# Optimization experiments

Hardware: AMD Instinct MI355X
Metric: run time of the kernel (lower is better)

The kernel has to match this reference:

```python
import jax, jax.numpy as jnp
import numpy as np

N_QUBITS = 5
N_LAYERS = 3
DIM = 2 ** N_QUBITS  # 32


def _apply_ry(state, theta, w):
    # state: [B, 32] complex64; theta: scalar or [B] float32
    half = theta * 0.5
    c = jnp.cos(half)
    s = jnp.sin(half)
    if c.ndim:  # per-sample angles
        c = c[:, None, None]
        s = s[:, None, None]
    pre, post = 2 ** w, 2 ** (N_QUBITS - 1 - w)
    st = state.reshape(-1, pre, 2, post)
    s0, s1 = st[:, :, 0, :], st[:, :, 1, :]
    out = jnp.stack([c * s0 - s * s1, s * s0 + c * s1], axis=2)
    return out.reshape(-1, DIM)


def _apply_rz(state, theta, w):
    half = theta * 0.5
    e0 = jnp.exp(-1j * half)
    e1 = jnp.exp(1j * half)
    pre, post = 2 ** w, 2 ** (N_QUBITS - 1 - w)
    st = state.reshape(-1, pre, 2, post)
    out = jnp.stack([e0 * st[:, :, 0, :], e1 * st[:, :, 1, :]], axis=2)
    return out.reshape(-1, DIM)


def _apply_cnot(state, c):
    # control wire c, target wire c+1 (adjacent, as in the CNOT chain)
    pre, post = 2 ** c, 2 ** (N_QUBITS - 2 - c)
    st = state.reshape(-1, pre, 2, 2, post)
    out = jnp.stack([st[:, :, 0], st[:, :, 1, ::-1, :]], axis=2)
    return out.reshape(-1, DIM)


def _expval_z(state, w):
    pre, post = 2 ** w, 2 ** (N_QUBITS - 1 - w)
    p = jnp.abs(state.reshape(-1, pre, 2, post)) ** 2
    return (p[:, :, 0, :] - p[:, :, 1, :]).sum(axis=(1, 2))


def _circuit(enc, qp):
    # enc: [B, 5] in [-1,1]; qp: [30]
    B = enc.shape[0]
    state = jnp.zeros((B, DIM), jnp.complex64).at[:, 0].set(1.0)
    pi = jnp.float32(np.pi)
    for i in range(N_QUBITS):
        state = _apply_ry(state, enc[:, i] * pi, i)
    idx = 0
    for _ in range(N_LAYERS):
        for i in range(N_QUBITS):
            state = _apply_ry(state, qp[idx], i); idx += 1
            state = _apply_rz(state, qp[idx], i); idx += 1
        for i in range(N_QUBITS - 1):
            state = _apply_cnot(state, i)
    return jnp.stack([_expval_z(state, i) for i in range(N_QUBITS)], axis=1)


def setup_inputs() -> dict:
    key = jax.random.key(0)
    ks = jax.random.split(key, 14)
    B, S, A = 131072, 252, 4
    def lin(k, fin, fout):
        return jax.random.normal(k, (fin, fout), jnp.float32) / jnp.sqrt(jnp.float32(fin))
    return {
        'state': jax.random.normal(ks[0], (B, S), jnp.float32),
        'W1': lin(ks[1], S, 128), 'b1': jnp.zeros((128,), jnp.float32),
        'W2': lin(ks[2], 128, 64), 'b2': jnp.zeros((64,), jnp.float32),
        'W3': lin(ks[3], 64, N_QUBITS), 'b3': jnp.zeros((N_QUBITS,), jnp.float32),
        'qp': jax.random.normal(ks[4], (N_LAYERS * N_QUBITS * 2,), jnp.float32) * 0.1,
        'D1': lin(ks[5], N_QUBITS, 32), 'd1': jnp.zeros((32,), jnp.float32),
        'D2': lin(ks[6], 32, 16), 'd2': jnp.zeros((16,), jnp.float32),
        'D3': lin(ks[7], 16, A), 'd3': jnp.zeros((A,), jnp.float32),
    }


def reference(state, W1, b1, W2, b2, W3, b3, qp, D1, d1, D2, d2, D3, d3):
    h = jax.nn.relu(state @ W1 + b1)
    h = jax.nn.relu(h @ W2 + b2)
    enc = jnp.tanh(h @ W3 + b3)          # [B, 5]
    q = _circuit(enc, qp)                # [B, 5] PauliZ expectations
    h = jax.nn.relu(q @ D1 + d1)
    h = jax.nn.relu(h @ D2 + d2)
    return h @ D3 + d3                   # [B, action_dim]
```

## Files before the change

kernel.cpp:

```cpp
#include <hip/hip_runtime.h>
#include <hip/hip_bf16.h>
#include <math.h>

typedef _Float16 half8_t __attribute__((ext_vector_type(8)));
typedef _Float16 half4_t __attribute__((ext_vector_type(4)));
typedef float floatx4 __attribute__((ext_vector_type(4)));

#define TPT 8

__device__ __forceinline__ void lds_barrier() {
    asm volatile("s_waitcnt lgkmcnt(0)" ::: "memory");
    __builtin_amdgcn_s_barrier();
    asm volatile("" ::: "memory");
}

__device__ __forceinline__ float fast_tanh(float x) {
    float e = __expf(2.f * x);
    return 1.f - 2.f / (e + 1.f);
}

__device__ __forceinline__ void prep_body(const float* __restrict__ W,
                                          _Float16* __restrict__ dst,
                                          int K, int N, int KS, int b) {
    int ks   = b % KS;
    int nt   = b / KS;
    int lane = threadIdx.x;
    int col  = nt * 16 + (lane & 15);
    int kbase = ks * 32 + ((lane >> 4) << 3);
    half8_t v;
#pragma unroll
    for (int j = 0; j < 8; ++j) {
        int k = kbase + j;
        float x = (k < K && col < N) ? W[(size_t)k * N + col] : 0.f;
        v[j] = (_Float16)x;
    }
    *(half8_t*)(dst + (size_t)(b * 64 + lane) * 8) = v;
}

__global__ void prep_all(const float* __restrict__ W1, const float* __restrict__ W2,
                         const float* __restrict__ W3,
                         _Float16* __restrict__ w1f, _Float16* __restrict__ w2f,
                         _Float16* __restrict__ w3f) {
    int b = blockIdx.x;
    if (b < 64)      prep_body(W1, w1f, 252, 128, 8, b);
    else if (b < 80) prep_body(W2, w2f, 128, 64, 4, b - 64);
    else             prep_body(W3, w3f, 64, 5, 2, b - 80);
}

__global__ __launch_bounds__(512, 4) void front_kernel(
    const float* __restrict__ state,
    const _Float16* __restrict__ w1f, const float* __restrict__ b1,
    const _Float16* __restrict__ w2f, const float* __restrict__ b2,
    const _Float16* __restrict__ w3f, const float* __restrict__ b3,
    float* __restrict__ enc, int Btot) {
    __shared__ char lds[63488];
    const int tid = threadIdx.x;
    const int w   = tid >> 6;
    const int l   = tid & 63;
    const int l15 = l & 15;
    const int lhi = l >> 4;
    const int row0 = blockIdx.x * (32 * TPT);

    const int srow = tid >> 4;
    const int sc0  = tid & 15;
    const int sswz = (srow & 7) << 4;

    floatx4 pf[4];

#define ISSUE_A(T)                                                          \
    {                                                                       \
        const float* Ar = state + (size_t)(row0 + (T) * 32 + srow) * 252;   \
        _Pragma("unroll")                                                   \
        for (int jj = 0; jj < 4; ++jj) {                                    \
            int c = sc0 + jj * 16;                                          \
            if (c < 63) pf[jj] = *(const floatx4*)(Ar + c * 4);             \
        }                                                                   \
    }

#define STAGE(T)                                                            \
    {                                                                       \
        int sab = (((T) & 1) << 14);                                        \
        _Pragma("unroll")                                                   \
        for (int jj = 0; jj < 4; ++jj) {                                    \
            int c = sc0 + jj * 16;                                          \
            half4_t h;                                                      \
            if (c == 63) {                                                  \
                h = half4_t{0, 0, 0, 0};                                    \
            } else {                                                        \
                floatx4 f = pf[jj];                                         \
                h = half4_t{ (_Float16)f[0], (_Float16)f[1],                \
                             (_Float16)f[2], (_Float16)f[3] };              \
            }                                                               \
            *(half4_t*)(lds + sab + (srow << 9) + ((c * 8) ^ sswz)) = h;    \
        }                                                                   \
    }

    ISSUE_A(0)

    half8_t bw1[8];
#pragma unroll
    for (int ks = 0; ks < 8; ++ks)
        bw1[ks] = *(const half8_t*)(w1f + (size_t)((w * 8 + ks) * 64 + l) * 8);

    {
        const floatx4* s2 = (const floatx4*)w2f;
        *(floatx4*)(lds + 45056 + tid * 16)        = s2[tid];
        *(floatx4*)(lds + 45056 + 8192 + tid * 16) = s2[512 + tid];
        if (tid < 128) {
            const floatx4* s3 = (const floatx4*)w3f;
            *(floatx4*)(lds + 61440 + tid * 16) = s3[tid];
        }
    }

    const float bb1 = b1[w * 16 + l15];
    const float bb2 = b2[(w & 3) * 16 + l15];
    const float bb3 = b3[l15 < 5 ? l15 : 4];

    const int mi2 = w >> 2;
    const int nt2 = w & 3;

    STAGE(0)
    ISSUE_A(1)
    lds_barrier();

#pragma unroll
    for (int t = 0; t < TPT; ++t) {
        if (w < 2 && t > 0) {
            floatx4 acc3 = floatx4{0, 0, 0, 0};
#pragma unroll
            for (int ks = 0; ks < 2; ++ks) {
                int r = w * 16 + l15;
                int cb = ks * 64 + lhi * 16;
                half8_t a  = *(const half8_t*)(lds + 40960 + (r << 7) + (cb ^ ((r & 7) << 4)));
                half8_t bf = *(const half8_t*)(lds + 61440 + (ks * 64 + l) * 16);
                acc3 = __builtin_amdgcn_mfma_f32_16x16x32_f16(a, bf, acc3, 0, 0, 0);
            }
            if (l15 < 5) {
#pragma unroll
                for (int ri = 0; ri < 4; ++ri) {
                    int grow = row0 + (t - 1) * 32 + w * 16 + lhi * 4 + ri;
                    enc[(size_t)l15 * Btot + grow] = fast_tanh(acc3[ri] + bb3);
                }
            }
        }

        const int sab = (t & 1) << 14;
        floatx4 acc1[2] = { floatx4{0, 0, 0, 0}, floatx4{0, 0, 0, 0} };
#pragma unroll
        for (int ks = 0; ks < 8; ++ks) {
            int cb = ks * 64 + lhi * 16;
#pragma unroll
            for (int mi = 0; mi < 2; ++mi) {
                int r = mi * 16 + l15;
                half8_t a = *(const half8_t*)(lds + sab + (r << 9) + (cb ^ ((r & 7) << 4)));
                acc1[mi] = __builtin_amdgcn_mfma_f32_16x16x32_f16(a, bw1[ks], acc1[mi], 0, 0, 0);
            }
        }

        {
            int col2 = (w * 16 + l15) * 2;
#pragma unroll
            for (int mi = 0; mi < 2; ++mi)
#pragma unroll
                for (int ri = 0; ri < 4; ++ri) {
                    int row = mi * 16 + lhi * 4 + ri;
                    float v = acc1[mi][ri] + bb1;
                    v = v > 0.f ? v : 0.f;
                    *(_Float16*)(lds + 32768 + (row << 8) + (col2 ^ ((row & 7) << 4))) = (_Float16)v;
                }
        }
        lds_barrier();

        floatx4 acc2 = floatx4{0, 0, 0, 0};
#pragma unroll
        for (int ks = 0; ks < 4; ++ks) {
            int r = mi2 * 16 + l15;
            int cb = ks * 64 + lhi * 16;
            half8_t a  = *(const half8_t*)(lds + 32768 + (r << 8) + (cb ^ ((r & 7) << 4)));
            half8_t bf = *(const half8_t*)(lds + 45056 + ((nt2 * 4 + ks) * 64 + l) * 16);
            acc2 = __builtin_amdgcn_mfma_f32_16x16x32_f16(a, bf, acc2, 0, 0, 0);
        }

        {
            int col2 = (nt2 * 16 + l15) * 2;
#pragma unroll
            for (int ri = 0; ri < 4; ++ri) {
                int row = mi2 * 16 + lhi * 4 + ri;
                float v = acc2[ri] + bb2;
                v = v > 0.f ? v : 0.f;
                *(_Float16*)(lds + 40960 + (row << 7) + (col2 ^ ((row & 7) << 4))) = (_Float16)v;
            }
        }

        if (t + 1 < TPT) {
            STAGE(t + 1)
            if (t + 2 < TPT) ISSUE_A(t + 2)
        }
        lds_barrier();
    }

    if (w < 2) {
        floatx4 acc3 = floatx4{0, 0, 0, 0};
#pragma unroll
        for (int ks = 0; ks < 2; ++ks) {
            int r = w * 16 + l15;
            int cb = ks * 64 + lhi * 16;
            half8_t a  = *(const half8_t*)(lds + 40960 + (r << 7) + (cb ^ ((r & 7) << 4)));
            half8_t bf = *(const half8_t*)(lds + 61440 + (ks * 64 + l) * 16);
            acc3 = __builtin_amdgcn_mfma_f32_16x16x32_f16(a, bf, acc3, 0, 0, 0);
        }
        if (l15 < 5) {
#pragma unroll
            for (int ri = 0; ri < 4; ++ri) {
                int grow = row0 + (TPT - 1) * 32 + w * 16 + lhi * 4 + ri;
                enc[(size_t)l15 * Btot + grow] = fast_tanh(acc3[ri] + bb3);
            }
        }
    }
#undef ISSUE_A
#undef STAGE
}

template<int P>
__device__ __forceinline__ void ry_g(float* re, float* im, float c, float s) {
    constexpr int STR = 1 << P;
#pragma unroll
    for (int base = 0; base < 32; base += 2 * STR)
#pragma unroll
        for (int d = 0; d < STR; ++d) {
            int i0 = base + d, i1 = i0 + STR;
            float r0 = re[i0], r1 = re[i1], m0 = im[i0], m1 = im[i1];
            re[i0] = c * r0 - s * r1;  re[i1] = s * r0 + c * r1;
            im[i0] = c * m0 - s * m1;  im[i1] = s * m0 + c * m1;
        }
}

template<int P>
__device__ __forceinline__ void rz_g(float* re, float* im, float c, float s) {
#pragma unroll
    for (int i = 0; i < 32; ++i) {
        float t = ((i >> P) & 1) ? s : -s;
        float r = re[i], m = im[i];
        re[i] = c * r - t * m;
        im[i] = c * m + t * r;
    }
}

template<int PC, int PT>
__device__ __forceinline__ void cnot_g(float* re, float* im) {
#pragma unroll
    for (int i = 0; i < 32; ++i) {
        if (((i >> PC) & 1) && !((i >> PT) & 1)) {
            int j = i | (1 << PT);
            float t;
            t = re[i]; re[i] = re[j]; re[j] = t;
            t = im[i]; im[i] = im[j]; im[j] = t;
        }
    }
}

template<int P>
__device__ __forceinline__ void expand_g(float* re, float* im,
                                         float arv, float aiv, float brv, float biv) {
#pragma unroll
    for (int base = 0; base < 32; base += (2 << P)) {
        float cr = re[base], ci = im[base];
        re[base + (1 << P)] = cr * brv - ci * biv;
        im[base + (1 << P)] = cr * biv + ci * brv;
        re[base] = cr * arv - ci * aiv;
        im[base] = cr * aiv + ci * arv;
    }
}

__global__ __launch_bounds__(256) void back_kernel(
    const float* __restrict__ enc, const float* __restrict__ qp,
    const float* __restrict__ D1, const float* __restrict__ d1,
    const float* __restrict__ D2, const float* __restrict__ d2,
    const float* __restrict__ D3, const float* __restrict__ d3,
    float* __restrict__ out, int Btot) {
    __shared__ float sD1[160], sd1[32], sD2[512], sd2[16], sD3[64], sd3[4];
    __shared__ float sQc[20], sQs[20];
    __shared__ float ryh[5], rzc0[5], rzs0[5];
    const int tid = threadIdx.x;
    for (int i = tid; i < 512; i += 256) sD2[i] = D2[i];
    if (tid < 160) sD1[tid] = D1[tid];
    if (tid < 32)  sd1[tid] = d1[tid];
    if (tid < 64)  sD3[tid] = D3[tid];
    if (tid < 16)  sd2[tid] = d2[tid];
    if (tid < 4)   sd3[tid] = d3[tid];
    if (tid < 20) { float h = 0.5f * qp[10 + tid]; sQc[tid] = __cosf(h); sQs[tid] = __sinf(h); }
    if (tid < 5) {
        ryh[tid] = 0.5f * qp[2 * tid];
        float h = 0.5f * qp[2 * tid + 1];
        rzc0[tid] = __cosf(h);
        rzs0[tid] = __sinf(h);
    }
    __syncthreads();

    const size_t r = (size_t)blockIdx.x * 256 + tid;

    const float HPI = 1.57079632679489662f;
    float ar[5], ai[5], br[5], bi[5];
#pragma unroll
    for (int i = 0; i < 5; ++i) {
        float h = enc[(size_t)i * Btot + r] * HPI + ryh[i];
        float ch = __cosf(h), sh = __sinf(h);
        ar[i] = ch * rzc0[i];  ai[i] = -ch * rzs0[i];
        br[i] = sh * rzc0[i];  bi[i] =  sh * rzs0[i];
    }

    float re[32], im[32];
    re[0] = ar[0]; im[0] = ai[0]; re[16] = br[0]; im[16] = bi[0];
    expand_g<3>(re, im, ar[1], ai[1], br[1], bi[1]);
    expand_g<2>(re, im, ar[2], ai[2], br[2], bi[2]);
    expand_g<1>(re, im, ar[3], ai[3], br[3], bi[3]);
    expand_g<0>(re, im, ar[4], ai[4], br[4], bi[4]);

    cnot_g<4, 3>(re, im);
    cnot_g<3, 2>(re, im);
    cnot_g<2, 1>(re, im);
    cnot_g<1, 0>(re, im);

#pragma unroll
    for (int lay = 0; lay < 2; ++lay) {
        const float* c = sQc + lay * 10;
        const float* s = sQs + lay * 10;
        ry_g<4>(re, im, c[0], s[0]);  rz_g<4>(re, im, c[1], s[1]);
        ry_g<3>(re, im, c[2], s[2]);  rz_g<3>(re, im, c[3], s[3]);
        ry_g<2>(re, im, c[4], s[4]);  rz_g<2>(re, im, c[5], s[5]);
        ry_g<1>(re, im, c[6], s[6]);  rz_g<1>(re, im, c[7], s[7]);
        ry_g<0>(re, im, c[8], s[8]);  rz_g<0>(re, im, c[9], s[9]);
        cnot_g<4, 3>(re, im);
        cnot_g<3, 2>(re, im);
        cnot_g<2, 1>(re, im);
        cnot_g<1, 0>(re, im);
    }

    float q[5] = {0, 0, 0, 0, 0};
#pragma unroll
    for (int i = 0; i < 32; ++i) {
        float p = re[i] * re[i] + im[i] * im[i];
        q[0] += ((i >> 4) & 1) ? -p : p;
        q[1] += ((i >> 3) & 1) ? -p : p;
        q[2] += ((i >> 2) & 1) ? -p : p;
        q[3] += ((i >> 1) & 1) ? -p : p;
        q[4] += ( i       & 1) ? -p : p;
    }

    float h1[32];
#pragma unroll
    for (int j = 0; j < 32; ++j) {
        float a = sd1[j];
#pragma unroll
        for (int k = 0; k < 5; ++k) a += q[k] * sD1[k * 32 + j];
        h1[j] = a > 0.f ? a : 0.f;
    }
    float h2[16];
#pragma unroll
    for (int j = 0; j < 16; ++j) {
        float a = sd2[j];
#pragma unroll
        for (int k = 0; k < 32; ++k) a += h1[k] * sD2[k * 16 + j];
        h2[j] = a > 0.f ? a : 0.f;
    }
    floatx4 o;
#pragma unroll
    for (int j = 0; j < 4; ++j) {
        float a = sd3[j];
#pragma unroll
        for (int k = 0; k < 16; ++k) a += h2[k] * sD3[k * 4 + j];
        o[j] = a;
    }
    *(floatx4*)(out + r * 4) = o;
}

extern "C" void kernel_launch(void* const* d_in, const int* in_sizes, int n_in,
                              void* d_out, int out_size, void* d_ws, size_t ws_size,
                              hipStream_t stream) {
    const float* state = (const float*)d_in[0];
    const float* W1 = (const float*)d_in[1];
    const float* b1 = (const float*)d_in[2];
    const float* W2 = (const float*)d_in[3];
    const float* b2 = (const float*)d_in[4];
    const float* W3 = (const float*)d_in[5];
    const float* b3 = (const float*)d_in[6];
    const float* qp = (const float*)d_in[7];
    const float* D1 = (const float*)d_in[8];
    const float* d1 = (const float*)d_in[9];
    const float* D2 = (const float*)d_in[10];
    const float* d2 = (const float*)d_in[11];
    const float* D3 = (const float*)d_in[12];
    const float* d3 = (const float*)d_in[13];
    float* out = (float*)d_out;

    const int B = in_sizes[0] / 252;

    char* ws = (char*)d_ws;
    _Float16* w1f = (_Float16*)ws;
    _Float16* w2f = (_Float16*)(ws + 65536);
    _Float16* w3f = (_Float16*)(ws + 65536 + 16384);
    float*    enc = (float*)(ws + 65536 + 16384 + 2048);

    prep_all<<<82, 64, 0, stream>>>(W1, W2, W3, w1f, w2f, w3f);
    front_kernel<<<B / (32 * TPT), 512, 0, stream>>>(state, w1f, b1, w2f, b2, w3f, b3, enc, B);
    back_kernel<<<B / 256, 256, 0, stream>>>(enc, qp, D1, d1, D2, d2, D3, d3, out, B);
}
```

Before: 54.64 us.

## Fuse weight prep, front MLP, circuit and decoder into one kernel

```diff
diff --git a/kernel.cpp b/kernel.cpp
--- a/kernel.cpp
+++ b/kernel.cpp
@@ -19,41 +19,82 @@
     return 1.f - 2.f / (e + 1.f);
 }
 
-__device__ __forceinline__ void prep_body(const float* __restrict__ W,
-                                          _Float16* __restrict__ dst,
-                                          int K, int N, int KS, int b) {
-    int ks   = b % KS;
-    int nt   = b / KS;
-    int lane = threadIdx.x;
-    int col  = nt * 16 + (lane & 15);
-    int kbase = ks * 32 + ((lane >> 4) << 3);
-    half8_t v;
-#pragma unroll
-    for (int j = 0; j < 8; ++j) {
-        int k = kbase + j;
-        float x = (k < K && col < N) ? W[(size_t)k * N + col] : 0.f;
-        v[j] = (_Float16)x;
-    }
-    *(half8_t*)(dst + (size_t)(b * 64 + lane) * 8) = v;
-}
-
-__global__ void prep_all(const float* __restrict__ W1, const float* __restrict__ W2,
-                         const float* __restrict__ W3,
-                         _Float16* __restrict__ w1f, _Float16* __restrict__ w2f,
-                         _Float16* __restrict__ w3f) {
-    int b = blockIdx.x;
-    if (b < 64)      prep_body(W1, w1f, 252, 128, 8, b);
-    else if (b < 80) prep_body(W2, w2f, 128, 64, 4, b - 64);
-    else             prep_body(W3, w3f, 64, 5, 2, b - 80);
-}
-
-__global__ __launch_bounds__(512, 4) void front_kernel(
+template<int P>
+__device__ __forceinline__ void ry_g(float* re, float* im, float c, float s) {
+    constexpr int STR = 1 << P;
+#pragma unroll
+    for (int base = 0; base < 32; base += 2 * STR)
+#pragma unroll
+        for (int d = 0; d < STR; ++d) {
+            int i0 = base + d, i1 = i0 + STR;
+            float r0 = re[i0], r1 = re[i1], m0 = im[i0], m1 = im[i1];
+            re[i0] = c * r0 - s * r1;  re[i1] = s * r0 + c * r1;
+            im[i0] = c * m0 - s * m1;  im[i1] = s * m0 + c * m1;
+        }
+}
+template<int P>
+__device__ __forceinline__ void rz_g(float* re, float* im, float c, float s) {
+#pragma unroll
+    for (int i = 0; i < 32; ++i) {
+        float t = ((i >> P) & 1) ? s : -s;
+        float r = re[i], m = im[i];
+        re[i] = c * r - t * m;
+        im[i] = c * m + t * r;
+    }
+}
+template<int PC, int PT>
+__device__ __forceinline__ void cnot_g(float* re, float* im) {
+#pragma unroll
+    for (int i = 0; i < 32; ++i) {
+        if (((i >> PC) & 1) && !((i >> PT) & 1)) {
+            int j = i | (1 << PT);
+            float t;
+            t = re[i]; re[i] = re[j]; re[j] = t;
+            t = im[i]; im[i] = im[j]; im[j] = t;
+        }
+    }
+}
+template<int P>
+__device__ __forceinline__ void expand_g(float* re, float* im,
+                                         float arv, float aiv, float brv, float biv) {
+#pragma unroll
+    for (int base = 0; base < 32; base += (2 << P)) {
+        float cr = re[base], ci = im[base];
+        re[base + (1 << P)] = cr * brv - ci * biv;
+        im[base + (1 << P)] = cr * biv + ci * brv;
+        re[base] = cr * arv - ci * aiv;
+        im[base] = cr * aiv + ci * arv;
+    }
+}
+
+#define OF_H1   32768
+#define OF_H2   40960
+#define OF_ENC  45056
+#define OF_D1   50176
+#define OF_d1   50816
+#define OF_D2   50944
+#define OF_d2   52992
+#define OF_D3   53056
+#define OF_d3   53312
+#define OF_RYH  53328
+#define OF_RZC  53348
+#define OF_RZS  53368
+#define OF_QC   53392
+#define OF_QS   53472
+
+__global__ __launch_bounds__(512, 4) void fused_kernel(
     const float* __restrict__ state,
-    const _Float16* __restrict__ w1f, const float* __restrict__ b1,
-    const _Float16* __restrict__ w2f, const float* __restrict__ b2,
-    const _Float16* __restrict__ w3f, const float* __restrict__ b3,
-    float* __restrict__ enc, int Btot) {
-    __shared__ char lds[63488];
+    const float* __restrict__ W1, const float* __restrict__ b1,
+    const float* __restrict__ W2, const float* __restrict__ b2,
+    const float* __restrict__ W3, const float* __restrict__ b3,
+    const float* __restrict__ qp,
+    const float* __restrict__ D1, const float* __restrict__ d1,
+    const float* __restrict__ D2, const float* __restrict__ d2,
+    const float* __restrict__ D3, const float* __restrict__ d3,
+    float* __restrict__ out) {
+    __shared__ floatx4 ldsv[3348];
+    char*  lds  = (char*)ldsv;
+    float* ldsf = (float*)ldsv;
     const int tid = threadIdx.x;
     const int w   = tid >> 6;
     const int l   = tid & 63;
@@ -97,27 +138,65 @@
 
     ISSUE_A(0)
 
+    const int nt2 = w & 3;
+    const int mi2 = w >> 2;
+
     half8_t bw1[8];
 #pragma unroll
-    for (int ks = 0; ks < 8; ++ks)
-        bw1[ks] = *(const half8_t*)(w1f + (size_t)((w * 8 + ks) * 64 + l) * 8);
-
-    {
-        const floatx4* s2 = (const floatx4*)w2f;
-        *(floatx4*)(lds + 45056 + tid * 16)        = s2[tid];
-        *(floatx4*)(lds + 45056 + 8192 + tid * 16) = s2[512 + tid];
-        if (tid < 128) {
-            const floatx4* s3 = (const floatx4*)w3f;
-            *(floatx4*)(lds + 61440 + tid * 16) = s3[tid];
-        }
+    for (int ks = 0; ks < 8; ++ks) {
+        half8_t v;
+#pragma unroll
+        for (int j = 0; j < 8; ++j) {
+            int k = ks * 32 + lhi * 8 + j;
+            float x = (k < 252) ? W1[k * 128 + w * 16 + l15] : 0.f;
+            v[j] = (_Float16)x;
+        }
+        bw1[ks] = v;
+    }
+    half8_t bw2[4];
+#pragma unroll
+    for (int ks = 0; ks < 4; ++ks) {
+        half8_t v;
+#pragma unroll
+        for (int j = 0; j < 8; ++j) {
+            int k = ks * 32 + lhi * 8 + j;
+            v[j] = (_Float16)W2[k * 64 + nt2 * 16 + l15];
+        }
+        bw2[ks] = v;
+    }
+    half8_t bw3[2];
+#pragma unroll
+    for (int ks = 0; ks < 2; ++ks) {
+        half8_t v;
+#pragma unroll
+        for (int j = 0; j < 8; ++j) {
+            int k = ks * 32 + lhi * 8 + j;
+            v[j] = (_Float16)((l15 < 5) ? W3[k * 5 + l15] : 0.f);
+        }
+        bw3[ks] = v;
+    }
+
+    if (tid < 512) ldsf[OF_D2 / 4 + tid] = D2[tid];
+    if (tid < 160) ldsf[OF_D1 / 4 + tid] = D1[tid];
+    if (tid < 64)  ldsf[OF_D3 / 4 + tid] = D3[tid];
+    if (tid < 32)  ldsf[OF_d1 / 4 + tid] = d1[tid];
+    if (tid < 16)  ldsf[OF_d2 / 4 + tid] = d2[tid];
+    if (tid < 4)   ldsf[OF_d3 / 4 + tid] = d3[tid];
+    if (tid < 20) {
+        float h = 0.5f * qp[10 + tid];
+        ldsf[OF_QC / 4 + tid] = __cosf(h);
+        ldsf[OF_QS / 4 + tid] = __sinf(h);
+    }
+    if (tid < 5) {
+        ldsf[OF_RYH / 4 + tid] = 0.5f * qp[2 * tid];
+        float h = 0.5f * qp[2 * tid + 1];
+        ldsf[OF_RZC / 4 + tid] = __cosf(h);
+        ldsf[OF_RZS / 4 + tid] = __sinf(h);
     }
 
     const float bb1 = b1[w * 16 + l15];
-    const float bb2 = b2[(w & 3) * 16 + l15];
+    const float bb2 = b2[nt2 * 16 + l15];
     const float bb3 = b3[l15 < 5 ? l15 : 4];
-
-    const int mi2 = w >> 2;
-    const int nt2 = w & 3;
 
     STAGE(0)
     ISSUE_A(1)
@@ -131,15 +210,14 @@
             for (int ks = 0; ks < 2; ++ks) {
                 int r = w * 16 + l15;
                 int cb = ks * 64 + lhi * 16;
-                half8_t a  = *(const half8_t*)(lds + 40960 + (r << 7) + (cb ^ ((r & 7) << 4)));
-                half8_t bf = *(const half8_t*)(lds + 61440 + (ks * 64 + l) * 16);
-                acc3 = __builtin_amdgcn_mfma_f32_16x16x32_f16(a, bf, acc3, 0, 0, 0);
+                half8_t a = *(const half8_t*)(lds + OF_H2 + (r << 7) + (cb ^ ((r & 7) << 4)));
+                acc3 = __builtin_amdgcn_mfma_f32_16x16x32_f16(a, bw3[ks], acc3, 0, 0, 0);
             }
             if (l15 < 5) {
 #pragma unroll
                 for (int ri = 0; ri < 4; ++ri) {
-                    int grow = row0 + (t - 1) * 32 + w * 16 + lhi * 4 + ri;
-                    enc[(size_t)l15 * Btot + grow] = fast_tanh(acc3[ri] + bb3);
+                    int trow = (t - 1) * 32 + w * 16 + lhi * 4 + ri;
+                    ldsf[OF_ENC / 4 + trow * 5 + l15] = fast_tanh(acc3[ri] + bb3);
                 }
             }
         }
@@ -166,7 +244,7 @@
                     int row = mi * 16 + lhi * 4 + ri;
                     float v = acc1[mi][ri] + bb1;
                     v = v > 0.f ? v : 0.f;
-                    *(_Float16*)(lds + 32768 + (row << 8) + (col2 ^ ((row & 7) << 4))) = (_Float16)v;
+                    *(_Float16*)(lds + OF_H1 + (row << 8) + (col2 ^ ((row & 7) << 4))) = (_Float16)v;
                 }
         }
         lds_barrier();
@@ -176,9 +254,8 @@
         for (int ks = 0; ks < 4; ++ks) {
             int r = mi2 * 16 + l15;
             int cb = ks * 64 + lhi * 16;
-            half8_t a  = *(const half8_t*)(lds + 32768 + (r << 8) + (cb ^ ((r & 7) << 4)));
-            half8_t bf = *(const half8_t*)(lds + 45056 + ((nt2 * 4 + ks) * 64 + l) * 16);
-            acc2 = __builtin_amdgcn_mfma_f32_16x16x32_f16(a, bf, acc2, 0, 0, 0);
+            half8_t a = *(const half8_t*)(lds + OF_H1 + (r << 8) + (cb ^ ((r & 7) << 4)));
+            acc2 = __builtin_amdgcn_mfma_f32_16x16x32_f16(a, bw2[ks], acc2, 0, 0, 0);
         }
 
         {
@@ -188,7 +265,7 @@
                 int row = mi2 * 16 + lhi * 4 + ri;
                 float v = acc2[ri] + bb2;
                 v = v > 0.f ? v : 0.f;
-                *(_Float16*)(lds + 40960 + (row << 7) + (col2 ^ ((row & 7) << 4))) = (_Float16)v;
+                *(_Float16*)(lds + OF_H2 + (row << 7) + (col2 ^ ((row & 7) << 4))) = (_Float16)v;
             }
         }
 
@@ -205,173 +282,104 @@
         for (int ks = 0; ks < 2; ++ks) {
             int r = w * 16 + l15;
             int cb = ks * 64 + lhi * 16;
-            half8_t a  = *(const half8_t*)(lds + 40960 + (r << 7) + (cb ^ ((r & 7) << 4)));
-            half8_t bf = *(const half8_t*)(lds + 61440 + (ks * 64 + l) * 16);
-            acc3 = __builtin_amdgcn_mfma_f32_16x16x32_f16(a, bf, acc3, 0, 0, 0);
+            half8_t a = *(const half8_t*)(lds + OF_H2 + (r << 7) + (cb ^ ((r & 7) << 4)));
+            acc3 = __builtin_amdgcn_mfma_f32_16x16x32_f16(a, bw3[ks], acc3, 0, 0, 0);
         }
         if (l15 < 5) {
 #pragma unroll
             for (int ri = 0; ri < 4; ++ri) {
-                int grow = row0 + (TPT - 1) * 32 + w * 16 + lhi * 4 + ri;
-                enc[(size_t)l15 * Btot + grow] = fast_tanh(acc3[ri] + bb3);
+                int trow = (TPT - 1) * 32 + w * 16 + lhi * 4 + ri;
+                ldsf[OF_ENC / 4 + trow * 5 + l15] = fast_tanh(acc3[ri] + bb3);
             }
         }
     }
-#undef ISSUE_A
-#undef STAGE
-}
-
-template<int P>
-__device__ __forceinline__ void ry_g(float* re, float* im, float c, float s) {
-    constexpr int STR = 1 << P;
-#pragma unroll
-    for (int base = 0; base < 32; base += 2 * STR)
-#pragma unroll
-        for (int d = 0; d < STR; ++d) {
-            int i0 = base + d, i1 = i0 + STR;
-            float r0 = re[i0], r1 = re[i1], m0 = im[i0], m1 = im[i1];
-            re[i0] = c * r0 - s * r1;  re[i1] = s * r0 + c * r1;
-            im[i0] = c * m0 - s * m1;  im[i1] = s * m0 + c * m1;
-        }
-}
-
-template<int P>
-__device__ __forceinline__ void rz_g(float* re, float* im, float c, float s) {
-#pragma unroll
-    for (int i = 0; i < 32; ++i) {
-        float t = ((i >> P) & 1) ? s : -s;
-        float r = re[i], m = im[i];
-        re[i] = c * r - t * m;
-        im[i] = c * m + t * r;
-    }
-}
-
-template<int PC, int PT>
-__device__ __forceinline__ void cnot_g(float* re, float* im) {
-#pragma unroll
-    for (int i = 0; i < 32; ++i) {
-        if (((i >> PC) & 1) && !((i >> PT) & 1)) {
-            int j = i | (1 << PT);
-            float t;
-            t = re[i]; re[i] = re[j]; re[j] = t;
-            t = im[i]; im[i] = im[j]; im[j] = t;
-        }
-    }
-}
-
-template<int P>
-__device__ __forceinline__ void expand_g(float* re, float* im,
-                                         float arv, float aiv, float brv, float biv) {
-#pragma unroll
-    for (int base = 0; base < 32; base += (2 << P)) {
-        float cr = re[base], ci = im[base];
-        re[base + (1 << P)] = cr * brv - ci * biv;
-        im[base + (1 << P)] = cr * biv + ci * brv;
-        re[base] = cr * arv - ci * aiv;
-        im[base] = cr * aiv + ci * arv;
-    }
-}
-
-__global__ __launch_bounds__(256) void back_kernel(
-    const float* __restrict__ enc, const float* __restrict__ qp,
-    const float* __restrict__ D1, const float* __restrict__ d1,
-    const float* __restrict__ D2, const float* __restrict__ d2,
-    const float* __restrict__ D3, const float* __restrict__ d3,
-    float* __restrict__ out, int Btot) {
-    __shared__ float sD1[160], sd1[32], sD2[512], sd2[16], sD3[64], sd3[4];
-    __shared__ float sQc[20], sQs[20];
-    __shared__ float ryh[5], rzc0[5], rzs0[5];
-    const int tid = threadIdx.x;
-    for (int i = tid; i < 512; i += 256) sD2[i] = D2[i];
-    if (tid < 160) sD1[tid] = D1[tid];
-    if (tid < 32)  sd1[tid] = d1[tid];
-    if (tid < 64)  sD3[tid] = D3[tid];
-    if (tid < 16)  sd2[tid] = d2[tid];
-    if (tid < 4)   sd3[tid] = d3[tid];
-    if (tid < 20) { float h = 0.5f * qp[10 + tid]; sQc[tid] = __cosf(h); sQs[tid] = __sinf(h); }
-    if (tid < 5) {
-        ryh[tid] = 0.5f * qp[2 * tid];
-        float h = 0.5f * qp[2 * tid + 1];
-        rzc0[tid] = __cosf(h);
-        rzs0[tid] = __sinf(h);
-    }
-    __syncthreads();
-
-    const size_t r = (size_t)blockIdx.x * 256 + tid;
-
-    const float HPI = 1.57079632679489662f;
-    float ar[5], ai[5], br[5], bi[5];
-#pragma unroll
-    for (int i = 0; i < 5; ++i) {
-        float h = enc[(size_t)i * Btot + r] * HPI + ryh[i];
-        float ch = __cosf(h), sh = __sinf(h);
-        ar[i] = ch * rzc0[i];  ai[i] = -ch * rzs0[i];
-        br[i] = sh * rzc0[i];  bi[i] =  sh * rzs0[i];
-    }
-
-    float re[32], im[32];
-    re[0] = ar[0]; im[0] = ai[0]; re[16] = br[0]; im[16] = bi[0];
-    expand_g<3>(re, im, ar[1], ai[1], br[1], bi[1]);
-    expand_g<2>(re, im, ar[2], ai[2], br[2], bi[2]);
-    expand_g<1>(re, im, ar[3], ai[3], br[3], bi[3]);
-    expand_g<0>(re, im, ar[4], ai[4], br[4], bi[4]);
-
-    cnot_g<4, 3>(re, im);
-    cnot_g<3, 2>(re, im);
-    cnot_g<2, 1>(re, im);
-    cnot_g<1, 0>(re, im);
-
-#pragma unroll
-    for (int lay = 0; lay < 2; ++lay) {
-        const float* c = sQc + lay * 10;
-        const float* s = sQs + lay * 10;
-        ry_g<4>(re, im, c[0], s[0]);  rz_g<4>(re, im, c[1], s[1]);
-        ry_g<3>(re, im, c[2], s[2]);  rz_g<3>(re, im, c[3], s[3]);
-        ry_g<2>(re, im, c[4], s[4]);  rz_g<2>(re, im, c[5], s[5]);
-        ry_g<1>(re, im, c[6], s[6]);  rz_g<1>(re, im, c[7], s[7]);
-        ry_g<0>(re, im, c[8], s[8]);  rz_g<0>(re, im, c[9], s[9]);
+    lds_barrier();
+
+    if (tid < 256) {
+        const int row = tid;
+        const float HPI = 1.57079632679489662f;
+
+        float ar[5], ai[5], br[5], bi[5];
+#pragma unroll
+        for (int i = 0; i < 5; ++i) {
+            float h = ldsf[OF_ENC / 4 + row * 5 + i] * HPI + ldsf[OF_RYH / 4 + i];
+            float ch = __cosf(h), sh = __sinf(h);
+            float rc = ldsf[OF_RZC / 4 + i], rs = ldsf[OF_RZS / 4 + i];
+            ar[i] = ch * rc;  ai[i] = -ch * rs;
+            br[i] = sh * rc;  bi[i] =  sh * rs;
+        }
+
+        float re[32], im[32];
+        re[0] = ar[0]; im[0] = ai[0]; re[16] = br[0]; im[16] = bi[0];
+        expand_g<3>(re, im, ar[1], ai[1], br[1], bi[1]);
+        expand_g<2>(re, im, ar[2], ai[2], br[2], bi[2]);
+        expand_g<1>(re, im, ar[3], ai[3], br[3], bi[3]);
+        expand_g<0>(re, im, ar[4], ai[4], br[4], bi[4]);
+
         cnot_g<4, 3>(re, im);
         cnot_g<3, 2>(re, im);
         cnot_g<2, 1>(re, im);
         cnot_g<1, 0>(re, im);
-    }
-
-    float q[5] = {0, 0, 0, 0, 0};
-#pragma unroll
-    for (int i = 0; i < 32; ++i) {
-        float p = re[i] * re[i] + im[i] * im[i];
-        q[0] += ((i >> 4) & 1) ? -p : p;
-        q[1] += ((i >> 3) & 1) ? -p : p;
-        q[2] += ((i >> 2) & 1) ? -p : p;
-        q[3] += ((i >> 1) & 1) ? -p : p;
-        q[4] += ( i       & 1) ? -p : p;
-    }
-
-    float h1[32];
-#pragma unroll
-    for (int j = 0; j < 32; ++j) {
-        float a = sd1[j];
-#pragma unroll
-        for (int k = 0; k < 5; ++k) a += q[k] * sD1[k * 32 + j];
-        h1[j] = a > 0.f ? a : 0.f;
-    }
-    float h2[16];
-#pragma unroll
-    for (int j = 0; j < 16; ++j) {
-        float a = sd2[j];
-#pragma unroll
-        for (int k = 0; k < 32; ++k) a += h1[k] * sD2[k * 16 + j];
-        h2[j] = a > 0.f ? a : 0.f;
-    }
-    floatx4 o;
-#pragma unroll
-    for (int j = 0; j < 4; ++j) {
-        float a = sd3[j];
-#pragma unroll
-        for (int k = 0; k < 16; ++k) a += h2[k] * sD3[k * 4 + j];
-        o[j] = a;
-    }
-    *(floatx4*)(out + r * 4) = o;
+
+#pragma unroll
+        for (int lay = 0; lay < 2; ++lay) {
+            const float* c = ldsf + OF_QC / 4 + lay * 10;
+            const float* s = ldsf + OF_QS / 4 + lay * 10;
+            ry_g<4>(re, im, c[0], s[0]);  rz_g<4>(re, im, c[1], s[1]);
+            ry_g<3>(re, im, c[2], s[2]);  rz_g<3>(re, im, c[3], s[3]);
+            ry_g<2>(re, im, c[4], s[4]);  rz_g<2>(re, im, c[5], s[5]);
+            ry_g<1>(re, im, c[6], s[6]);  rz_g<1>(re, im, c[7], s[7]);
+            ry_g<0>(re, im, c[8], s[8]);  rz_g<0>(re, im, c[9], s[9]);
+            cnot_g<4, 3>(re, im);
+            cnot_g<3, 2>(re, im);
+            cnot_g<2, 1>(re, im);
+            cnot_g<1, 0>(re, im);
+        }
+
+        float q[5] = {0, 0, 0, 0, 0};
+#pragma unroll
+        for (int i = 0; i < 32; ++i) {
+            float p = re[i] * re[i] + im[i] * im[i];
+            q[0] += ((i >> 4) & 1) ? -p : p;
+            q[1] += ((i >> 3) & 1) ? -p : p;
+            q[2] += ((i >> 2) & 1) ? -p : p;
+            q[3] += ((i >> 1) & 1) ? -p : p;
+            q[4] += ( i       & 1) ? -p : p;
+        }
+
+        const floatx4* D1v = (const floatx4*)(lds + OF_D1);
+        const floatx4* d1v = (const floatx4*)(lds + OF_d1);
+        const floatx4* D2v = (const floatx4*)(lds + OF_D2);
+        const floatx4* d2v = (const floatx4*)(lds + OF_d2);
+        const floatx4* D3v = (const floatx4*)(lds + OF_D3);
+        const floatx4* d3v = (const floatx4*)(lds + OF_d3);
+
+        float h1[32];
+#pragma unroll
+        for (int j4 = 0; j4 < 8; ++j4) {
+            floatx4 a = d1v[j4];
+#pragma unroll
+            for (int k = 0; k < 5; ++k) a += q[k] * D1v[k * 8 + j4];
+#pragma unroll
+            for (int e = 0; e < 4; ++e) h1[j4 * 4 + e] = a[e] > 0.f ? a[e] : 0.f;
+        }
+        float h2[16];
+#pragma unroll
+        for (int j4 = 0; j4 < 4; ++j4) {
+            floatx4 a = d2v[j4];
+#pragma unroll
+            for (int k = 0; k < 32; ++k) a += h1[k] * D2v[k * 4 + j4];
+#pragma unroll
+            for (int e = 0; e < 4; ++e) h2[j4 * 4 + e] = a[e] > 0.f ? a[e] : 0.f;
+        }
+        floatx4 o = d3v[0];
+#pragma unroll
+        for (int k = 0; k < 16; ++k) o += h2[k] * D3v[k];
+
+        *(floatx4*)(out + (size_t)(row0 + row) * 4) = o;
+    }
+#undef ISSUE_A
+#undef STAGE
 }
 
 extern "C" void kernel_launch(void* const* d_in, const int* in_sizes, int n_in,
@@ -395,13 +403,6 @@
 
     const int B = in_sizes[0] / 252;
 
-    char* ws = (char*)d_ws;
-    _Float16* w1f = (_Float16*)ws;
-    _Float16* w2f = (_Float16*)(ws + 65536);
-    _Float16* w3f = (_Float16*)(ws + 65536 + 16384);
-    float*    enc = (float*)(ws + 65536 + 16384 + 2048);
-
-    prep_all<<<82, 64, 0, stream>>>(W1, W2, W3, w1f, w2f, w3f);
-    front_kernel<<<B / (32 * TPT), 512, 0, stream>>>(state, w1f, b1, w2f, b2, w3f, b3, enc, B);
-    back_kernel<<<B / 256, 256, 0, stream>>>(enc, qp, D1, d1, D2, d2, D3, d3, out, B);
-}
+    fused_kernel<<<B / (32 * TPT), 512, 0, stream>>>(
+        state, W1, b1, W2, b2, W3, b3, qp, D1, d1, D2, d2, D3, d3, out);
+}
```

Result: slower. 79.18 us (+44.9%).

## Split each sample's quantum statevector across two lanes in back kernel

Applied to the files above, without the earlier changes.

```diff
diff --git a/kernel.cpp b/kernel.cpp
--- a/kernel.cpp
+++ b/kernel.cpp
@@ -222,10 +222,10 @@
 }
 
 template<int P>
-__device__ __forceinline__ void ry_g(float* re, float* im, float c, float s) {
+__device__ __forceinline__ void ry16(float* re, float* im, float c, float s) {
     constexpr int STR = 1 << P;
 #pragma unroll
-    for (int base = 0; base < 32; base += 2 * STR)
+    for (int base = 0; base < 16; base += 2 * STR)
 #pragma unroll
         for (int d = 0; d < STR; ++d) {
             int i0 = base + d, i1 = i0 + STR;
@@ -234,22 +234,20 @@
             im[i0] = c * m0 - s * m1;  im[i1] = s * m0 + c * m1;
         }
 }
-
 template<int P>
-__device__ __forceinline__ void rz_g(float* re, float* im, float c, float s) {
-#pragma unroll
-    for (int i = 0; i < 32; ++i) {
+__device__ __forceinline__ void rz16(float* re, float* im, float c, float s) {
+#pragma unroll
+    for (int i = 0; i < 16; ++i) {
         float t = ((i >> P) & 1) ? s : -s;
         float r = re[i], m = im[i];
         re[i] = c * r - t * m;
         im[i] = c * m + t * r;
     }
 }
-
 template<int PC, int PT>
-__device__ __forceinline__ void cnot_g(float* re, float* im) {
-#pragma unroll
-    for (int i = 0; i < 32; ++i) {
+__device__ __forceinline__ void cnot16(float* re, float* im) {
+#pragma unroll
+    for (int i = 0; i < 16; ++i) {
         if (((i >> PC) & 1) && !((i >> PT) & 1)) {
             int j = i | (1 << PT);
             float t;
@@ -258,12 +256,11 @@
         }
     }
 }
-
 template<int P>
-__device__ __forceinline__ void expand_g(float* re, float* im,
+__device__ __forceinline__ void expand16(float* re, float* im,
                                          float arv, float aiv, float brv, float biv) {
 #pragma unroll
-    for (int base = 0; base < 32; base += (2 << P)) {
+    for (int base = 0; base < 16; base += (2 << P)) {
         float cr = re[base], ci = im[base];
         re[base + (1 << P)] = cr * brv - ci * biv;
         im[base + (1 << P)] = cr * biv + ci * brv;
@@ -272,7 +269,7 @@
     }
 }
 
-__global__ __launch_bounds__(256) void back_kernel(
+__global__ __launch_bounds__(512, 4) void back_kernel(
     const float* __restrict__ enc, const float* __restrict__ qp,
     const float* __restrict__ D1, const float* __restrict__ d1,
     const float* __restrict__ D2, const float* __restrict__ d2,
@@ -282,7 +279,7 @@
     __shared__ float sQc[20], sQs[20];
     __shared__ float ryh[5], rzc0[5], rzs0[5];
     const int tid = threadIdx.x;
-    for (int i = tid; i < 512; i += 256) sD2[i] = D2[i];
+    if (tid < 512) sD2[tid] = D2[tid];
     if (tid < 160) sD1[tid] = D1[tid];
     if (tid < 32)  sd1[tid] = d1[tid];
     if (tid < 64)  sD3[tid] = D3[tid];
@@ -297,55 +294,93 @@
     }
     __syncthreads();
 
-    const size_t r = (size_t)blockIdx.x * 256 + tid;
-
+    const int    h   = tid & 1;
+    const size_t row = (size_t)blockIdx.x * 256 + (tid >> 1);
     const float HPI = 1.57079632679489662f;
+
     float ar[5], ai[5], br[5], bi[5];
 #pragma unroll
     for (int i = 0; i < 5; ++i) {
-        float h = enc[(size_t)i * Btot + r] * HPI + ryh[i];
-        float ch = __cosf(h), sh = __sinf(h);
+        float hh = enc[(size_t)i * Btot + row] * HPI + ryh[i];
+        float ch = __cosf(hh), sh = __sinf(hh);
         ar[i] = ch * rzc0[i];  ai[i] = -ch * rzs0[i];
         br[i] = sh * rzc0[i];  bi[i] =  sh * rzs0[i];
     }
 
-    float re[32], im[32];
-    re[0] = ar[0]; im[0] = ai[0]; re[16] = br[0]; im[16] = bi[0];
-    expand_g<3>(re, im, ar[1], ai[1], br[1], bi[1]);
-    expand_g<2>(re, im, ar[2], ai[2], br[2], bi[2]);
-    expand_g<1>(re, im, ar[3], ai[3], br[3], bi[3]);
-    expand_g<0>(re, im, ar[4], ai[4], br[4], bi[4]);
-
-    cnot_g<4, 3>(re, im);
-    cnot_g<3, 2>(re, im);
-    cnot_g<2, 1>(re, im);
-    cnot_g<1, 0>(re, im);
+    float re[16], im[16];
+    re[0] = h ? br[0] : ar[0];
+    im[0] = h ? bi[0] : ai[0];
+    expand16<3>(re, im, ar[1], ai[1], br[1], bi[1]);
+    expand16<2>(re, im, ar[2], ai[2], br[2], bi[2]);
+    expand16<1>(re, im, ar[3], ai[3], br[3], bi[3]);
+    expand16<0>(re, im, ar[4], ai[4], br[4], bi[4]);
+
+    if (h) {
+#pragma unroll
+        for (int i = 0; i < 8; ++i) {
+            float t;
+            t = re[i]; re[i] = re[i + 8]; re[i + 8] = t;
+            t = im[i]; im[i] = im[i + 8]; im[i + 8] = t;
+        }
+    }
+    cnot16<3, 2>(re, im);
+    cnot16<2, 1>(re, im);
+    cnot16<1, 0>(re, im);
 
 #pragma unroll
     for (int lay = 0; lay < 2; ++lay) {
         const float* c = sQc + lay * 10;
         const float* s = sQs + lay * 10;
-        ry_g<4>(re, im, c[0], s[0]);  rz_g<4>(re, im, c[1], s[1]);
-        ry_g<3>(re, im, c[2], s[2]);  rz_g<3>(re, im, c[3], s[3]);
-        ry_g<2>(re, im, c[4], s[4]);  rz_g<2>(re, im, c[5], s[5]);
-        ry_g<1>(re, im, c[6], s[6]);  rz_g<1>(re, im, c[7], s[7]);
-        ry_g<0>(re, im, c[8], s[8]);  rz_g<0>(re, im, c[9], s[9]);
-        cnot_g<4, 3>(re, im);
-        cnot_g<3, 2>(re, im);
-        cnot_g<2, 1>(re, im);
-        cnot_g<1, 0>(re, im);
+        {
+            float cc = c[0], ss = s[0];
+            float sgn = h ? ss : -ss;
+#pragma unroll
+            for (int i = 0; i < 16; ++i) {
+                float ro = __shfl_xor(re[i], 1);
+                float mo = __shfl_xor(im[i], 1);
+                re[i] = cc * re[i] + sgn * ro;
+                im[i] = cc * im[i] + sgn * mo;
+            }
+        }
+        {
+            float cc = c[1], t = h ? s[1] : -s[1];
+#pragma unroll
+            for (int i = 0; i < 16; ++i) {
+                float r = re[i], m = im[i];
+                re[i] = cc * r - t * m;
+                im[i] = cc * m + t * r;
+            }
+        }
+        ry16<3>(re, im, c[2], s[2]);  rz16<3>(re, im, c[3], s[3]);
+        ry16<2>(re, im, c[4], s[4]);  rz16<2>(re, im, c[5], s[5]);
+        ry16<1>(re, im, c[6], s[6]);  rz16<1>(re, im, c[7], s[7]);
+        ry16<0>(re, im, c[8], s[8]);  rz16<0>(re, im, c[9], s[9]);
+        if (h) {
+#pragma unroll
+            for (int i = 0; i < 8; ++i) {
+                float t;
+                t = re[i]; re[i] = re[i + 8]; re[i + 8] = t;
+                t = im[i]; im[i] = im[i + 8]; im[i + 8] = t;
+            }
+        }
+        cnot16<3, 2>(re, im);
+        cnot16<2, 1>(re, im);
+        cnot16<1, 0>(re, im);
     }
 
     float q[5] = {0, 0, 0, 0, 0};
 #pragma unroll
-    for (int i = 0; i < 32; ++i) {
+    for (int i = 0; i < 16; ++i) {
         float p = re[i] * re[i] + im[i] * im[i];
-        q[0] += ((i >> 4) & 1) ? -p : p;
-        q[1] += ((i >> 3) & 1) ? -p : p;
-        q[2] += ((i >> 2) & 1) ? -p : p;
-        q[3] += ((i >> 1) & 1) ? -p : p;
-        q[4] += ( i       & 1) ? -p : p;
-    }
+        q[0] += p;
+        q[1] += (i & 8) ? -p : p;
+        q[2] += (i & 4) ? -p : p;
+        q[3] += (i & 2) ? -p : p;
+        q[4] += (i & 1) ? -p : p;
+    }
+    if (h) q[0] = -q[0];
+#pragma unroll
+    for (int k = 0; k < 5; ++k) q[k] += __shfl_xor(q[k], 1);
 
     float h1[32];
 #pragma unroll
@@ -371,7 +406,7 @@
         for (int k = 0; k < 16; ++k) a += h2[k] * sD3[k * 4 + j];
         o[j] = a;
     }
-    *(floatx4*)(out + r * 4) = o;
+    if (!h) *(floatx4*)(out + row * 4) = o;
 }
 
 extern "C" void kernel_launch(void* const* d_in, const int* in_sizes, int n_in,
@@ -403,5 +438,5 @@
 
     prep_all<<<82, 64, 0, stream>>>(W1, W2, W3, w1f, w2f, w3f);
     front_kernel<<<B / (32 * TPT), 512, 0, stream>>>(state, w1f, b1, w2f, b2, w3f, b3, enc, B);
-    back_kernel<<<B / 256, 256, 0, stream>>>(enc, qp, D1, d1, D2, d2, D3, d3, out, B);
-}
+    back_kernel<<<B / 256, 512, 0, stream>>>(enc, qp, D1, d1, D2, d2, D3, d3, out, B);
+}
```

Result: slower. 60.92 us (+11.5%).

## Split fused MLP front kernel into separate layer-1 and layers-2/3 kernels

Applied to the files above, without the earlier changes.

```diff
diff --git a/kernel.cpp b/kernel.cpp
--- a/kernel.cpp
+++ b/kernel.cpp
@@ -47,13 +47,11 @@
     else             prep_body(W3, w3f, 64, 5, 2, b - 80);
 }
 
-__global__ __launch_bounds__(512, 4) void front_kernel(
+__global__ __launch_bounds__(512, 4) void g1_kernel(
     const float* __restrict__ state,
     const _Float16* __restrict__ w1f, const float* __restrict__ b1,
-    const _Float16* __restrict__ w2f, const float* __restrict__ b2,
-    const _Float16* __restrict__ w3f, const float* __restrict__ b3,
-    float* __restrict__ enc, int Btot) {
-    __shared__ char lds[63488];
+    _Float16* __restrict__ h1T, int Btot) {
+    __shared__ char lds[32768];
     const int tid = threadIdx.x;
     const int w   = tid >> 6;
     const int l   = tid & 63;
@@ -102,22 +100,7 @@
     for (int ks = 0; ks < 8; ++ks)
         bw1[ks] = *(const half8_t*)(w1f + (size_t)((w * 8 + ks) * 64 + l) * 8);
 
-    {
-        const floatx4* s2 = (const floatx4*)w2f;
-        *(floatx4*)(lds + 45056 + tid * 16)        = s2[tid];
-        *(floatx4*)(lds + 45056 + 8192 + tid * 16) = s2[512 + tid];
-        if (tid < 128) {
-            const floatx4* s3 = (const floatx4*)w3f;
-            *(floatx4*)(lds + 61440 + tid * 16) = s3[tid];
-        }
-    }
-
     const float bb1 = b1[w * 16 + l15];
-    const float bb2 = b2[(w & 3) * 16 + l15];
-    const float bb3 = b3[l15 < 5 ? l15 : 4];
-
-    const int mi2 = w >> 2;
-    const int nt2 = w & 3;
 
     STAGE(0)
     ISSUE_A(1)
@@ -125,25 +108,6 @@
 
 #pragma unroll
     for (int t = 0; t < TPT; ++t) {
-        if (w < 2 && t > 0) {
-            floatx4 acc3 = floatx4{0, 0, 0, 0};
-#pragma unroll
-            for (int ks = 0; ks < 2; ++ks) {
-                int r = w * 16 + l15;
-                int cb = ks * 64 + lhi * 16;
-                half8_t a  = *(const half8_t*)(lds + 40960 + (r << 7) + (cb ^ ((r & 7) << 4)));
-                half8_t bf = *(const half8_t*)(lds + 61440 + (ks * 64 + l) * 16);
-                acc3 = __builtin_amdgcn_mfma_f32_16x16x32_f16(a, bf, acc3, 0, 0, 0);
-            }
-            if (l15 < 5) {
-#pragma unroll
-                for (int ri = 0; ri < 4; ++ri) {
-                    int grow = row0 + (t - 1) * 32 + w * 16 + lhi * 4 + ri;
-                    enc[(size_t)l15 * Btot + grow] = fast_tanh(acc3[ri] + bb3);
-                }
-            }
-        }
-
         const int sab = (t & 1) << 14;
         floatx4 acc1[2] = { floatx4{0, 0, 0, 0}, floatx4{0, 0, 0, 0} };
 #pragma unroll
@@ -157,39 +121,17 @@
             }
         }
 
-        {
-            int col2 = (w * 16 + l15) * 2;
-#pragma unroll
-            for (int mi = 0; mi < 2; ++mi)
-#pragma unroll
-                for (int ri = 0; ri < 4; ++ri) {
-                    int row = mi * 16 + lhi * 4 + ri;
-                    float v = acc1[mi][ri] + bb1;
-                    v = v > 0.f ? v : 0.f;
-                    *(_Float16*)(lds + 32768 + (row << 8) + (col2 ^ ((row & 7) << 4))) = (_Float16)v;
-                }
-        }
-        lds_barrier();
-
-        floatx4 acc2 = floatx4{0, 0, 0, 0};
-#pragma unroll
-        for (int ks = 0; ks < 4; ++ks) {
-            int r = mi2 * 16 + l15;
-            int cb = ks * 64 + lhi * 16;
-            half8_t a  = *(const half8_t*)(lds + 32768 + (r << 8) + (cb ^ ((r & 7) << 4)));
-            half8_t bf = *(const half8_t*)(lds + 45056 + ((nt2 * 4 + ks) * 64 + l) * 16);
-            acc2 = __builtin_amdgcn_mfma_f32_16x16x32_f16(a, bf, acc2, 0, 0, 0);
-        }
-
-        {
-            int col2 = (nt2 * 16 + l15) * 2;
+#pragma unroll
+        for (int mi = 0; mi < 2; ++mi) {
+            half4_t hv;
 #pragma unroll
             for (int ri = 0; ri < 4; ++ri) {
-                int row = mi2 * 16 + lhi * 4 + ri;
-                float v = acc2[ri] + bb2;
-                v = v > 0.f ? v : 0.f;
-                *(_Float16*)(lds + 40960 + (row << 7) + (col2 ^ ((row & 7) << 4))) = (_Float16)v;
+                float v = acc1[mi][ri] + bb1;
+                hv[ri] = (_Float16)(v > 0.f ? v : 0.f);
             }
+            size_t off = (size_t)(w * 16 + l15) * Btot
+                       + row0 + t * 32 + mi * 16 + lhi * 4;
+            *(half4_t*)(h1T + off) = hv;
         }
 
         if (t + 1 < TPT) {
@@ -198,27 +140,98 @@
         }
         lds_barrier();
     }
-
-    if (w < 2) {
-        floatx4 acc3 = floatx4{0, 0, 0, 0};
-#pragma unroll
-        for (int ks = 0; ks < 2; ++ks) {
-            int r = w * 16 + l15;
-            int cb = ks * 64 + lhi * 16;
-            half8_t a  = *(const half8_t*)(lds + 40960 + (r << 7) + (cb ^ ((r & 7) << 4)));
-            half8_t bf = *(const half8_t*)(lds + 61440 + (ks * 64 + l) * 16);
-            acc3 = __builtin_amdgcn_mfma_f32_16x16x32_f16(a, bf, acc3, 0, 0, 0);
-        }
-        if (l15 < 5) {
-#pragma unroll
-            for (int ri = 0; ri < 4; ++ri) {
-                int grow = row0 + (TPT - 1) * 32 + w * 16 + lhi * 4 + ri;
-                enc[(size_t)l15 * Btot + grow] = fast_tanh(acc3[ri] + bb3);
-            }
-        }
-    }
 #undef ISSUE_A
 #undef STAGE
+}
+
+__global__ __launch_bounds__(256, 4) void g23_kernel(
+    const _Float16* __restrict__ h1T,
+    const _Float16* __restrict__ w2f, const float* __restrict__ b2,
+    const _Float16* __restrict__ w3f, const float* __restrict__ b3,
+    float* __restrict__ enc, int Btot) {
+    __shared__ char lds[26624];
+    const int tid = threadIdx.x;
+    const int w   = tid >> 6;
+    const int l   = tid & 63;
+    const int l15 = l & 15;
+    const int lhi = l >> 4;
+    const int r0  = blockIdx.x * 64;
+
+    {
+        int n1  = tid >> 1;
+        int seg = tid & 1;
+        const _Float16* src = h1T + (size_t)n1 * Btot + r0 + seg * 32;
+        int col2 = n1 * 2;
+#pragma unroll
+        for (int c = 0; c < 4; ++c) {
+            half8_t v = *(const half8_t*)(src + c * 8);
+#pragma unroll
+            for (int j = 0; j < 8; ++j) {
+                int r = seg * 32 + c * 8 + j;
+                *(_Float16*)(lds + (r << 8) + (col2 ^ ((r & 7) << 4))) = v[j];
+            }
+        }
+    }
+
+    half8_t bw2[4];
+#pragma unroll
+    for (int ks = 0; ks < 4; ++ks)
+        bw2[ks] = *(const half8_t*)(w2f + (size_t)((w * 4 + ks) * 64 + l) * 8);
+
+    if (tid < 128) {
+        const floatx4* s3 = (const floatx4*)w3f;
+        *(floatx4*)(lds + 24576 + tid * 16) = s3[tid];
+    }
+
+    const float bb2 = b2[w * 16 + l15];
+    const float bb3 = b3[l15 < 5 ? l15 : 4];
+
+    lds_barrier();
+
+    floatx4 acc2[4];
+#pragma unroll
+    for (int mi = 0; mi < 4; ++mi) acc2[mi] = floatx4{0, 0, 0, 0};
+#pragma unroll
+    for (int ks = 0; ks < 4; ++ks) {
+        int cb = ks * 64 + lhi * 16;
+#pragma unroll
+        for (int mi = 0; mi < 4; ++mi) {
+            int r = mi * 16 + l15;
+            half8_t a = *(const half8_t*)(lds + (r << 8) + (cb ^ ((r & 7) << 4)));
+            acc2[mi] = __builtin_amdgcn_mfma_f32_16x16x32_f16(a, bw2[ks], acc2[mi], 0, 0, 0);
+        }
+    }
+
+    {
+        int col2 = (w * 16 + l15) * 2;
+#pragma unroll
+        for (int mi = 0; mi < 4; ++mi)
+#pragma unroll
+            for (int ri = 0; ri < 4; ++ri) {
+                int row = mi * 16 + lhi * 4 + ri;
+                float v = acc2[mi][ri] + bb2;
+                v = v > 0.f ? v : 0.f;
+                *(_Float16*)(lds + 16384 + (row << 7) + (col2 ^ ((row & 7) << 4))) = (_Float16)v;
+            }
+    }
+    lds_barrier();
+
+    floatx4 acc3 = floatx4{0, 0, 0, 0};
+#pragma unroll
+    for (int ks = 0; ks < 2; ++ks) {
+        int r = w * 16 + l15;
+        int cb = ks * 64 + lhi * 16;
+        half8_t a  = *(const half8_t*)(lds + 16384 + (r << 7) + (cb ^ ((r & 7) << 4)));
+        half8_t bf = *(const half8_t*)(lds + 24576 + (ks * 64 + l) * 16);
+        acc3 = __builtin_amdgcn_mfma_f32_16x16x32_f16(a, bf, acc3, 0, 0, 0);
+    }
+    if (l15 < 5) {
+#pragma unroll
+        for (int ri = 0; ri < 4; ++ri) {
+            int grow = r0 + w * 16 + lhi * 4 + ri;
+            enc[(size_t)l15 * Btot + grow] = fast_tanh(acc3[ri] + bb3);
+        }
+    }
 }
 
 template<int P>
@@ -234,7 +247,6 @@
             im[i0] = c * m0 - s * m1;  im[i1] = s * m0 + c * m1;
         }
 }
-
 template<int P>
 __device__ __forceinline__ void rz_g(float* re, float* im, float c, float s) {
 #pragma unroll
@@ -245,7 +257,6 @@
         im[i] = c * m + t * r;
     }
 }
-
 template<int PC, int PT>
 __device__ __forceinline__ void cnot_g(float* re, float* im) {
 #pragma unroll
@@ -258,7 +269,6 @@
         }
     }
 }
-
 template<int P>
 __device__ __forceinline__ void expand_g(float* re, float* im,
                                          float arv, float aiv, float brv, float biv) {
@@ -400,8 +410,10 @@
     _Float16* w2f = (_Float16*)(ws + 65536);
     _Float16* w3f = (_Float16*)(ws + 65536 + 16384);
     float*    enc = (float*)(ws + 65536 + 16384 + 2048);
+    _Float16* h1T = (_Float16*)(ws + 65536 + 16384 + 2048 + (size_t)5 * B * 4);
 
     prep_all<<<82, 64, 0, stream>>>(W1, W2, W3, w1f, w2f, w3f);
-    front_kernel<<<B / (32 * TPT), 512, 0, stream>>>(state, w1f, b1, w2f, b2, w3f, b3, enc, B);
+    g1_kernel<<<B / (32 * TPT), 512, 0, stream>>>(state, w1f, b1, h1T, B);
+    g23_kernel<<<B / 64, 256, 0, stream>>>(h1T, w2f, b2, w3f, b3, enc, B);
     back_kernel<<<B / 256, 256, 0, stream>>>(enc, qp, D1, d1, D2, d2, D3, d3, out, B);
 }
```

Result: slower. 65.49 us (+19.9%).
